# Performance work log

Measured on AMD Instinct MI355X. Metric: run time of the kernel, lower is better.

The kernel has to match this reference:

```python
import jax, jax.numpy as jnp
import numpy as np

TOK, B, DIM, TXT, NT, KS, H = 576, 64, 1024, 512, 1000, 3, 24
SCALE = TXT ** -0.5  # qk_scale = head_dim**-0.5 with head_dim = out_dim = 512


def _layernorm(x, g, b, eps=1e-5):
    m = jnp.mean(x, axis=-1, keepdims=True)
    v = jnp.var(x, axis=-1, keepdims=True)
    return (x - m) * jax.lax.rsqrt(v + eps) * g + b


def _cross_attn(q_in, kv, Wq):
    # q_in: [B,tok,DIM] -> q: [B,tok,TXT]; kv: [B,NT,TXT] serves as both K and V
    q = jnp.einsum('btd,de->bte', q_in, Wq)
    attn = jax.nn.softmax(jnp.einsum('bte,bne->btn', q, kv) * SCALE, axis=-1)
    return jnp.einsum('btn,bne->bte', attn, kv)


def _dwconv(z, w):
    # z: [B,1,H,H], w: [1,1,KS,KS], padding KS//2, stride 1
    return jax.lax.conv_general_dilated(
        z, w, window_strides=(1, 1), padding=((KS // 2, KS // 2), (KS // 2, KS // 2)),
        dimension_numbers=('NCHW', 'OIHW', 'NCHW'))


def setup_inputs() -> dict:
    key = jax.random.key(0)
    ks = jax.random.split(key, 6)
    return {
        'x': jax.random.normal(ks[0], (TOK + 1, B, DIM), jnp.float32),
        'text_fea': jax.random.normal(ks[1], (NT, B, TXT), jnp.float32),
        'ln_q1_g': jnp.ones((DIM,), jnp.float32), 'ln_q1_b': jnp.zeros((DIM,), jnp.float32),
        'ln_q2_g': jnp.ones((DIM,), jnp.float32), 'ln_q2_b': jnp.zeros((DIM,), jnp.float32),
        'ln_kv_g': jnp.ones((TXT,), jnp.float32), 'ln_kv_b': jnp.zeros((TXT,), jnp.float32),
        'Wq1': jax.random.normal(ks[2], (DIM, TXT), jnp.float32) * 0.02,
        'Wq2': jax.random.normal(ks[3], (DIM, TXT), jnp.float32) * 0.02,
        'conv_dw': jax.random.normal(ks[4], (1, 1, KS, KS), jnp.float32) * 0.1,
        'conv_final': jax.random.normal(ks[5], (DIM, TXT), jnp.float32) * 0.02,  # [out,in]
    }


def reference(x, text_fea, ln_q1_g, ln_q1_b, ln_q2_g, ln_q2_b, ln_kv_g, ln_kv_b,
              Wq1, Wq2, conv_dw, conv_final):
    x_cls, xp = x[:1], x[1:]                      # [1,B,DIM], [TOK,B,DIM]
    x_loc = jnp.transpose(xp, (1, 0, 2))          # [B,TOK,DIM]
    kv = _layernorm(jnp.transpose(text_fea, (1, 0, 2)), ln_kv_g, ln_kv_b)  # [B,NT,TXT]

    o1 = _cross_attn(_layernorm(x_loc, ln_q1_g, ln_q1_b), kv, Wq1)  # [B,TOK,TXT]
    o2 = _cross_attn(_layernorm(x_loc, ln_q2_g, ln_q2_b), kv, Wq2)

    x1 = jnp.transpose(o1, (0, 2, 1)).reshape(B, TXT, H, H)
    x2 = jnp.transpose(o2, (0, 2, 1)).reshape(B, TXT, H, H)

    avg_x = jnp.mean(x1, axis=1, keepdims=True)   # [B,1,H,H]
    max_x = jnp.max(x2, axis=1, keepdims=True)
    gate1 = jax.nn.sigmoid(_dwconv(avg_x, conv_dw))
    gate2 = jax.nn.sigmoid(_dwconv(max_x, conv_dw))

    x_se = x1 * gate1 + x2 * gate2                # [B,TXT,H,H]
    y = jnp.einsum('bchw,oc->bohw', x_se, conv_final)  # 1x1 conv, padding 0

    y = jnp.transpose(y.reshape(B, DIM, TOK), (2, 0, 1))  # [TOK,B,DIM]
    return jnp.concatenate([x_cls, y], axis=0)
```

## Files before the change

kernel.cpp:

```cpp
#include <hip/hip_runtime.h>

#define B_    64
#define TOK_  576
#define DIM_  1024
#define TXT_  512
#define NT_   1000
#define NTQ_  1024
#define NTP_  1024
#define H_    24
#define BT_   (B_ * TOK_)
static constexpr float SCALE_ = 0.0441941738241592f;

typedef __bf16 bf16x8 __attribute__((ext_vector_type(8)));
typedef float  f32x4  __attribute__((ext_vector_type(4)));

__device__ __forceinline__ unsigned short f2bf(float f) {
    unsigned u = __float_as_uint(f);
    u += 0x7fffu + ((u >> 16) & 1u);
    return (unsigned short)(u >> 16);
}
__device__ __forceinline__ float bf2f(unsigned short h) {
    return __uint_as_float(((unsigned)h) << 16);
}
__device__ __forceinline__ f32x4 mfma16(bf16x8 a, bf16x8 b, f32x4 c) {
    return __builtin_amdgcn_mfma_f32_16x16x32_bf16(a, b, c, 0, 0, 0);
}
__device__ __forceinline__ void unpack8(uint4 v, float* f) {
    unsigned a0 = v.x, a1 = v.y, a2 = v.z, a3 = v.w;
    f[0] = bf2f((unsigned short)(a0 & 0xffff)); f[1] = bf2f((unsigned short)(a0 >> 16));
    f[2] = bf2f((unsigned short)(a1 & 0xffff)); f[3] = bf2f((unsigned short)(a1 >> 16));
    f[4] = bf2f((unsigned short)(a2 & 0xffff)); f[5] = bf2f((unsigned short)(a2 >> 16));
    f[6] = bf2f((unsigned short)(a3 & 0xffff)); f[7] = bf2f((unsigned short)(a3 >> 16));
}

typedef const __attribute__((address_space(1))) unsigned int* as1_u32p;
typedef __attribute__((address_space(3))) unsigned int* as3_u32p;
__device__ __forceinline__ void gll16(const void* g, void* l) {
    __builtin_amdgcn_global_load_lds((as1_u32p)g, (as3_u32p)l, 16, 0, 0);
}

__global__ void k_prep_wq(const float* __restrict__ wq1, const float* __restrict__ wq2,
                          const float* __restrict__ g1, const float* __restrict__ g2,
                          unsigned short* __restrict__ wqt) {
    __shared__ float tile[64][68];
    int bx = blockIdx.x, t = threadIdx.x;
    int br = bx >> 7, kt = (bx >> 3) & 15, nt = bx & 7;
    const float* wq = br ? wq2 : wq1;
    const float* gg = br ? g2 : g1;
#pragma unroll
    for (int i = 0; i < 4; ++i) {
        int idx4 = t + i * 256;
        int kl = idx4 >> 4, n4 = (idx4 & 15) * 4;
        float gv = gg[kt * 64 + kl];
        float4 v = *reinterpret_cast<const float4*>(wq + (size_t)(kt * 64 + kl) * 512 + nt * 64 + n4);
        tile[kl][n4 + 0] = v.x * gv; tile[kl][n4 + 1] = v.y * gv;
        tile[kl][n4 + 2] = v.z * gv; tile[kl][n4 + 3] = v.w * gv;
    }
    __syncthreads();
#pragma unroll
    for (int i = 0; i < 4; ++i) {
        int idx4 = t + i * 256;
        int nl = idx4 >> 4, k4 = (idx4 & 15) * 4;
        ushort4 o = make_ushort4(f2bf(tile[k4 + 0][nl]), f2bf(tile[k4 + 1][nl]),
                                 f2bf(tile[k4 + 2][nl]), f2bf(tile[k4 + 3][nl]));
        *reinterpret_cast<ushort4*>(wqt + (size_t)br * 512 * 1024 + (size_t)(nt * 64 + nl) * 1024 + kt * 64 + k4) = o;
    }
}

__global__ void k_qbias(const float* __restrict__ wq1, const float* __restrict__ wq2,
                        const float* __restrict__ b1, const float* __restrict__ b2,
                        float* __restrict__ qbias) {
    int br = blockIdx.x >> 3, e0 = (blockIdx.x & 7) * 64;
    int t = threadIdx.x;
    int e = e0 + (t & 63), part = t >> 6;
    const float* wq = br ? wq2 : wq1;
    const float* bb = br ? b2 : b1;
    float s = 0.f;
    for (int d = part * 256; d < part * 256 + 256; ++d) s += bb[d] * wq[(size_t)d * 512 + e];
    __shared__ float red[256];
    red[t] = s;
    __syncthreads();
    if (t < 64) qbias[br * 512 + e0 + t] = red[t] + red[64 + t] + red[128 + t] + red[192 + t];
}

__global__ void k_f2bf(const float* __restrict__ src, unsigned short* __restrict__ dst, int n4) {
    int i = blockIdx.x * blockDim.x + threadIdx.x;
    if (i < n4) {
        float4 v = *reinterpret_cast<const float4*>(src + (size_t)i * 4);
        ushort4 o = make_ushort4(f2bf(v.x), f2bf(v.y), f2bf(v.z), f2bf(v.w));
        *reinterpret_cast<ushort4*>(dst + (size_t)i * 4) = o;
    }
}

__global__ void k_kvln(const float* __restrict__ tf, const float* __restrict__ g,
                       const float* __restrict__ bta, unsigned short* __restrict__ kvn) {
    int row = blockIdx.x;
    int b = row >> 10, n = row & 1023;
    int t = threadIdx.x;
    unsigned short* dst = kvn + ((size_t)b * NTQ_ + n) * TXT_;
    if (n >= NT_) {
        *reinterpret_cast<ushort4*>(dst + t * 4) = make_ushort4(0, 0, 0, 0);
        return;
    }
    const float* src = tf + ((size_t)n * B_ + b) * TXT_;
    float4 v = *reinterpret_cast<const float4*>(src + t * 4);
    float s = v.x + v.y + v.z + v.w;
    float ss = v.x * v.x + v.y * v.y + v.z * v.z + v.w * v.w;
#pragma unroll
    for (int d = 1; d < 64; d <<= 1) { s += __shfl_xor(s, d); ss += __shfl_xor(ss, d); }
    __shared__ float red[4];
    if ((t & 63) == 0) { red[(t >> 6) * 2] = s; red[(t >> 6) * 2 + 1] = ss; }
    __syncthreads();
    s = red[0] + red[2]; ss = red[1] + red[3];
    float m = s * (1.f / TXT_);
    float rs = rsqrtf(ss * (1.f / TXT_) - m * m + 1e-5f);
    int d0 = t * 4;
    ushort4 o = make_ushort4(f2bf((v.x - m) * rs * g[d0 + 0] + bta[d0 + 0]),
                             f2bf((v.y - m) * rs * g[d0 + 1] + bta[d0 + 1]),
                             f2bf((v.z - m) * rs * g[d0 + 2] + bta[d0 + 2]),
                             f2bf((v.w - m) * rs * g[d0 + 3] + bta[d0 + 3]));
    *reinterpret_cast<ushort4*>(dst + d0) = o;
}

__global__ void k_kvt(const unsigned short* __restrict__ kvn, unsigned short* __restrict__ kvt) {
    __shared__ unsigned short tile[64][68];
    int bx = blockIdx.x;
    int b = bx >> 7, rem = bx & 127, et = rem >> 4, nt = rem & 15;
    int t = threadIdx.x;
#pragma unroll
    for (int i = 0; i < 4; ++i) {
        int idx4 = t + i * 256;
        int nl = idx4 >> 4, e4 = (idx4 & 15) * 4;
        int ng = nt * 64 + nl;
        ushort4 v = make_ushort4(0, 0, 0, 0);
        if (ng < NT_) v = *reinterpret_cast<const ushort4*>(kvn + ((size_t)b * NTQ_ + ng) * TXT_ + et * 64 + e4);
        tile[nl][e4 + 0] = v.x; tile[nl][e4 + 1] = v.y; tile[nl][e4 + 2] = v.z; tile[nl][e4 + 3] = v.w;
    }
    __syncthreads();
#pragma unroll
    for (int i = 0; i < 4; ++i) {
        int idx4 = t + i * 256;
        int el = idx4 >> 4, n4 = (idx4 & 15) * 4;
        ushort4 o = make_ushort4(tile[n4 + 0][el], tile[n4 + 1][el], tile[n4 + 2][el], tile[n4 + 3][el]);
        *reinterpret_cast<ushort4*>(kvt + ((size_t)b * TXT_ + et * 64 + el) * NTP_ + nt * 64 + n4) = o;
    }
}

__global__ void k_xln(const float* __restrict__ x, unsigned short* __restrict__ xn) {
    int bt = blockIdx.x;
    int b = bt / TOK_, tk = bt - b * TOK_;
    const float* src = x + ((size_t)(tk + 1) * B_ + b) * DIM_;
    int t = threadIdx.x;
    float4 v = *reinterpret_cast<const float4*>(src + t * 4);
    float s = v.x + v.y + v.z + v.w;
    float ss = v.x * v.x + v.y * v.y + v.z * v.z + v.w * v.w;
#pragma unroll
    for (int d = 1; d < 64; d <<= 1) { s += __shfl_xor(s, d); ss += __shfl_xor(ss, d); }
    __shared__ float red[8];
    if ((t & 63) == 0) { red[t >> 6] = s; red[4 + (t >> 6)] = ss; }
    __syncthreads();
    s = red[0] + red[1] + red[2] + red[3];
    ss = red[4] + red[5] + red[6] + red[7];
    float m = s * (1.f / DIM_);
    float rs = rsqrtf(ss * (1.f / DIM_) - m * m + 1e-5f);
    int d0 = t * 4;
    ushort4 o = make_ushort4(f2bf((v.x - m) * rs), f2bf((v.y - m) * rs),
                             f2bf((v.z - m) * rs), f2bf((v.w - m) * rs));
    *reinterpret_cast<ushort4*>(xn + (size_t)bt * DIM_ + d0) = o;
}

__device__ __forceinline__ void gemm_loop_gll(const unsigned short* __restrict__ A,
                                              const unsigned short* __restrict__ Bp,
                                              int K, unsigned short* a_lds, unsigned short* b_lds,
                                              int tid, f32x4 acc[4][4]) {
    const int l = tid & 63, w = tid >> 6;
    const int l16 = l & 15, lg = l >> 4;
    const int wm = w & 1, wn = w >> 1;
    const f32x4 fz = {0.f, 0.f, 0.f, 0.f};
#pragma unroll
    for (int mt = 0; mt < 4; ++mt)
#pragma unroll
        for (int nt = 0; nt < 4; ++nt) acc[mt][nt] = fz;
    const int lrow = l >> 3;
    const int k8g = (l & 7) ^ lrow;
    const int nk = K >> 6;
    for (int kt = 0; kt < nk; ++kt) {
#pragma unroll
        for (int i = 0; i < 4; ++i) {
            int row = i * 32 + w * 8 + lrow;
            gll16(A + (size_t)row * K + kt * 64 + k8g * 8, &a_lds[(i * 256 + w * 64) * 8]);
        }
#pragma unroll
        for (int i = 0; i < 4; ++i) {
            int row = i * 32 + w * 8 + lrow;
            gll16(Bp + (size_t)row * K + kt * 64 + k8g * 8, &b_lds[(i * 256 + w * 64) * 8]);
        }
        __syncthreads();
#pragma unroll
        for (int kk = 0; kk < 2; ++kk) {
            bf16x8 af[4], bff[4];
#pragma unroll
            for (int mt = 0; mt < 4; ++mt) {
                int row = wm * 64 + mt * 16 + l16;
                int gs = (kk * 4 + lg) ^ (row & 7);
                af[mt] = *reinterpret_cast<const bf16x8*>(a_lds + row * 64 + gs * 8);
            }
#pragma unroll
            for (int nt = 0; nt < 4; ++nt) {
                int row = wn * 64 + nt * 16 + l16;
                int gs = (kk * 4 + lg) ^ (row & 7);
                bff[nt] = *reinterpret_cast<const bf16x8*>(b_lds + row * 64 + gs * 8);
            }
#pragma unroll
            for (int mt = 0; mt < 4; ++mt)
#pragma unroll
                for (int nt = 0; nt < 4; ++nt)
                    acc[mt][nt] = mfma16(af[mt], bff[nt], acc[mt][nt]);
        }
        __syncthreads();
    }
}

__device__ __forceinline__ void gemm_loop96(const unsigned short* __restrict__ A,
                                            const unsigned short* __restrict__ Bp,
                                            int K, unsigned short* a_lds, unsigned short* b_lds,
                                            int tid, f32x4 acc[3][4]) {
    const int l = tid & 63, w = tid >> 6;
    const int l16 = l & 15, lg = l >> 4;
    const int wm = w & 1, wn = w >> 1;
    const f32x4 fz = {0.f, 0.f, 0.f, 0.f};
#pragma unroll
    for (int mt = 0; mt < 3; ++mt)
#pragma unroll
        for (int nt = 0; nt < 4; ++nt) acc[mt][nt] = fz;
    const int lrow = l >> 3;
    const int k8g = (l & 7) ^ lrow;
    const int nk = K >> 6;
    for (int kt = 0; kt < nk; ++kt) {
#pragma unroll
        for (int i = 0; i < 3; ++i) {
            int row = i * 32 + w * 8 + lrow;
            gll16(A + (size_t)row * K + kt * 64 + k8g * 8, &a_lds[(i * 256 + w * 64) * 8]);
        }
#pragma unroll
        for (int i = 0; i < 4; ++i) {
            int row = i * 32 + w * 8 + lrow;
            gll16(Bp + (size_t)row * K + kt * 64 + k8g * 8, &b_lds[(i * 256 + w * 64) * 8]);
        }
        __syncthreads();
#pragma unroll
        for (int kk = 0; kk < 2; ++kk) {
            bf16x8 af[3], bff[4];
#pragma unroll
            for (int mt = 0; mt < 3; ++mt) {
                int row = wm * 48 + mt * 16 + l16;
                int gs = (kk * 4 + lg) ^ (row & 7);
                af[mt] = *reinterpret_cast<const bf16x8*>(a_lds + row * 64 + gs * 8);
            }
#pragma unroll
            for (int nt = 0; nt < 4; ++nt) {
                int row = wn * 64 + nt * 16 + l16;
                int gs = (kk * 4 + lg) ^ (row & 7);
                bff[nt] = *reinterpret_cast<const bf16x8*>(b_lds + row * 64 + gs * 8);
            }
#pragma unroll
            for (int mt = 0; mt < 3; ++mt)
#pragma unroll
                for (int nt = 0; nt < 4; ++nt)
                    acc[mt][nt] = mfma16(af[mt], bff[nt], acc[mt][nt]);
        }
        __syncthreads();
    }
}

__global__ __launch_bounds__(256, 4) void k_qgemm(const unsigned short* __restrict__ xn,
                                                  const unsigned short* __restrict__ wqt,
                                                  const float* __restrict__ qbias,
                                                  unsigned short* __restrict__ qb) {
    int bid = blockIdx.x;
    int vb = (bid & 7) * 288 + (bid >> 3);
    int bn = vb & 3;
    int t = vb >> 2;
    int br = (t >= 288) ? 1 : 0;
    int bm = t - br * 288;
    const unsigned short* A = xn + (size_t)bm * 128 * DIM_;
    const unsigned short* Bp = wqt + (size_t)br * 512 * 1024 + (size_t)bn * 128 * 1024;
    unsigned short* C = qb + (size_t)br * BT_ * TXT_;
    const float* bias = qbias + br * 512;
    __shared__ unsigned short a_lds[128 * 64];
    __shared__ unsigned short b_lds[128 * 64];
    f32x4 acc[4][4];
    gemm_loop_gll(A, Bp, DIM_, a_lds, b_lds, threadIdx.x, acc);
    const int l = threadIdx.x & 63, w = threadIdx.x >> 6;
    const int l16 = l & 15, lg = l >> 4, wm = w & 1, wn = w >> 1;
#pragma unroll
    for (int mt = 0; mt < 4; ++mt)
#pragma unroll
        for (int nt = 0; nt < 4; ++nt) {
            int col = bn * 128 + wn * 64 + nt * 16 + l16;
            float bv = bias[col];
#pragma unroll
            for (int r = 0; r < 4; ++r) {
                int row = bm * 128 + wm * 64 + mt * 16 + lg * 4 + r;
                C[(size_t)row * TXT_ + col] = f2bf((acc[mt][nt][r] + bv) * SCALE_);
            }
        }
}

__global__ __launch_bounds__(256, 4) void k_score(const unsigned short* __restrict__ qbuf,
                                                  const unsigned short* __restrict__ kvn,
                                                  unsigned short* __restrict__ P,
                                                  float* __restrict__ denom, int br) {
    int bid = blockIdx.x;
    int vb = (bid & 7) * 384 + (bid >> 3);
    int tile = vb % 48, b = vb / 48;
    int mt = tile >> 3, nt = tile & 7;
    const unsigned short* A = qbuf + ((size_t)br * BT_ + (size_t)b * TOK_ + mt * 96) * TXT_;
    const unsigned short* Bp = kvn + (size_t)b * NTQ_ * TXT_ + (size_t)nt * 128 * TXT_;
    __shared__ unsigned short a_lds[96 * 64];
    __shared__ unsigned short b_lds[128 * 64];
    f32x4 acc[3][4];
    gemm_loop96(A, Bp, TXT_, a_lds, b_lds, threadIdx.x, acc);
    const int l = threadIdx.x & 63, w = threadIdx.x >> 6;
    const int l16 = l & 15, lg = l >> 4, wm = w & 1, wn = w >> 1;
    float* dn = denom + (size_t)br * BT_;
#pragma unroll
    for (int mt2 = 0; mt2 < 3; ++mt2)
#pragma unroll
        for (int r = 0; r < 4; ++r) {
            int row = b * TOK_ + mt * 96 + wm * 48 + mt2 * 16 + lg * 4 + r;
            float s = 0.f;
#pragma unroll
            for (int nt2 = 0; nt2 < 4; ++nt2) {
                int col = nt * 128 + wn * 64 + nt2 * 16 + l16;
                float p = (col < NT_) ? __expf(acc[mt2][nt2][r]) : 0.f;
                s += p;
                P[(size_t)row * NTP_ + col] = f2bf(p);
            }
#pragma unroll
            for (int d = 1; d < 16; d <<= 1) s += __shfl_xor(s, d);
            if (l16 == 0) atomicAdd(&dn[row], s);
        }
}

__global__ __launch_bounds__(256, 4) void k_pv(const unsigned short* __restrict__ P,
                                               const unsigned short* __restrict__ kvt,
                                               const float* __restrict__ denom,
                                               unsigned short* __restrict__ ob, int br) {
    int bid = blockIdx.x;
    int vb = (bid & 7) * 192 + (bid >> 3);
    int tile = vb % 24, b = vb / 24;
    int mt = tile >> 2, nt = tile & 3;
    const unsigned short* A = P + ((size_t)b * TOK_ + mt * 96) * NTP_;
    const unsigned short* Bp = kvt + (size_t)b * TXT_ * NTP_ + (size_t)nt * 128 * NTP_;
    __shared__ unsigned short a_lds[96 * 64];
    __shared__ unsigned short b_lds[128 * 64];
    f32x4 acc[3][4];
    gemm_loop96(A, Bp, NTP_, a_lds, b_lds, threadIdx.x, acc);
    const int l = threadIdx.x & 63, w = threadIdx.x >> 6;
    const int l16 = l & 15, lg = l >> 4, wm = w & 1, wn = w >> 1;
    const float* dn = denom + (size_t)br * BT_;
#pragma unroll
    for (int mt2 = 0; mt2 < 3; ++mt2)
#pragma unroll
        for (int r = 0; r < 4; ++r) {
            int row = b * TOK_ + mt * 96 + wm * 48 + mt2 * 16 + lg * 4 + r;
            float inv = 1.f / dn[row];
            unsigned short* dst = ob + ((size_t)br * BT_ + row) * TXT_;
#pragma unroll
            for (int nt2 = 0; nt2 < 4; ++nt2) {
                int col = nt * 128 + wn * 64 + nt2 * 16 + l16;
                dst[col] = f2bf(acc[mt2][nt2][r] * inv);
            }
        }
}

__global__ __launch_bounds__(256, 4) void k_fgemm(const unsigned short* __restrict__ xse,
                                                  const unsigned short* __restrict__ wfb,
                                                  float* __restrict__ out) {
    int bid = blockIdx.x;
    int vb = (bid & 7) * 288 + (bid >> 3);
    int bn = vb & 7, bm = vb >> 3;
    const unsigned short* A = xse + (size_t)bm * 128 * TXT_;
    const unsigned short* Bp = wfb + (size_t)bn * 128 * TXT_;
    __shared__ unsigned short a_lds[128 * 64];
    __shared__ unsigned short b_lds[128 * 64];
    f32x4 acc[4][4];
    gemm_loop_gll(A, Bp, TXT_, a_lds, b_lds, threadIdx.x, acc);
    const int l = threadIdx.x & 63, w = threadIdx.x >> 6;
    const int l16 = l & 15, lg = l >> 4, wm = w & 1, wn = w >> 1;
#pragma unroll
    for (int mt = 0; mt < 4; ++mt)
#pragma unroll
        for (int r = 0; r < 4; ++r) {
            int rowg = bm * 128 + wm * 64 + mt * 16 + lg * 4 + r;
            int b = rowg / TOK_, tk = rowg - b * TOK_;
            float* dst = out + ((size_t)(tk + 1) * B_ + b) * DIM_;
#pragma unroll
            for (int nt = 0; nt < 4; ++nt) {
                int col = bn * 128 + wn * 64 + nt * 16 + l16;
                dst[col] = acc[mt][nt][r];
            }
        }
}

__global__ void k_avgmax(const unsigned short* __restrict__ o1, const unsigned short* __restrict__ o2,
                         float* __restrict__ avgb, float* __restrict__ maxb) {
    int row = blockIdx.x * 4 + (threadIdx.x >> 6);
    int l = threadIdx.x & 63;
    float f[8];
    unpack8(*reinterpret_cast<const uint4*>(o1 + (size_t)row * TXT_ + l * 8), f);
    float s = f[0] + f[1] + f[2] + f[3] + f[4] + f[5] + f[6] + f[7];
    unpack8(*reinterpret_cast<const uint4*>(o2 + (size_t)row * TXT_ + l * 8), f);
    float mx = f[0];
#pragma unroll
    for (int j = 1; j < 8; ++j) mx = fmaxf(mx, f[j]);
#pragma unroll
    for (int d = 1; d < 64; d <<= 1) { s += __shfl_xor(s, d); mx = fmaxf(mx, __shfl_xor(mx, d)); }
    if (l == 0) { avgb[row] = s * (1.f / TXT_); maxb[row] = mx; }
}

__global__ void k_gate(const float* __restrict__ avgb, const float* __restrict__ maxb,
                       const float* __restrict__ cdw, float* __restrict__ g1, float* __restrict__ g2) {
    int idx = blockIdx.x * 256 + threadIdx.x;
    int b = idx / TOK_, hw = idx - b * TOK_, h = hw / H_, ww = hw - h * H_;
    float a1 = 0.f, a2 = 0.f;
#pragma unroll
    for (int ky = 0; ky < 3; ++ky)
#pragma unroll
        for (int kx = 0; kx < 3; ++kx) {
            int hh = h + ky - 1, wx = ww + kx - 1;
            if (hh >= 0 && hh < H_ && wx >= 0 && wx < H_) {
                float wv = cdw[ky * 3 + kx];
                int s = b * TOK_ + hh * H_ + wx;
                a1 += wv * avgb[s];
                a2 += wv * maxb[s];
            }
        }
    g1[idx] = 1.f / (1.f + __expf(-a1));
    g2[idx] = 1.f / (1.f + __expf(-a2));
}

__global__ void k_xse(const unsigned short* __restrict__ o1, const unsigned short* __restrict__ o2,
                      const float* __restrict__ g1, const float* __restrict__ g2,
                      unsigned short* __restrict__ xse) {
    int idx8 = blockIdx.x * 256 + threadIdx.x;
    int bt = idx8 >> 6, e8 = idx8 & 63;
    float f1[8], f2[8];
    unpack8(*reinterpret_cast<const uint4*>(o1 + (size_t)bt * TXT_ + e8 * 8), f1);
    unpack8(*reinterpret_cast<const uint4*>(o2 + (size_t)bt * TXT_ + e8 * 8), f2);
    float gg1 = g1[bt], gg2 = g2[bt];
    unsigned r[4];
#pragma unroll
    for (int j = 0; j < 4; ++j) {
        unsigned lo = f2bf(f1[2 * j] * gg1 + f2[2 * j] * gg2);
        unsigned hi = f2bf(f1[2 * j + 1] * gg1 + f2[2 * j + 1] * gg2);
        r[j] = lo | (hi << 16);
    }
    uint4 o = make_uint4(r[0], r[1], r[2], r[3]);
    *reinterpret_cast<uint4*>(xse + (size_t)bt * TXT_ + e8 * 8) = o;
}

extern "C" void kernel_launch(void* const* d_in, const int* in_sizes, int n_in,
                              void* d_out, int out_size, void* d_ws, size_t ws_size,
                              hipStream_t stream) {
    (void)in_sizes; (void)n_in; (void)out_size; (void)ws_size;
    const float* x    = (const float*)d_in[0];
    const float* tf   = (const float*)d_in[1];
    const float* lq1g = (const float*)d_in[2];
    const float* lq1b = (const float*)d_in[3];
    const float* lq2g = (const float*)d_in[4];
    const float* lq2b = (const float*)d_in[5];
    const float* lkvg = (const float*)d_in[6];
    const float* lkvb = (const float*)d_in[7];
    const float* wq1  = (const float*)d_in[8];
    const float* wq2  = (const float*)d_in[9];
    const float* cdw  = (const float*)d_in[10];
    const float* wf   = (const float*)d_in[11];
    float* out = (float*)d_out;

    char* ws = (char*)d_ws;
    size_t off = 0;
    auto carve = [&](size_t bytes) { char* p = ws + off; off += (bytes + 255) & ~(size_t)255; return p; };
    unsigned short* kvn  = (unsigned short*)carve((size_t)B_ * NTQ_ * TXT_ * 2);
    unsigned short* kvt  = (unsigned short*)carve((size_t)B_ * TXT_ * NTP_ * 2);
    unsigned short* wqt  = (unsigned short*)carve((size_t)2 * 512 * 1024 * 2);
    unsigned short* wfb  = (unsigned short*)carve((size_t)1024 * 512 * 2);
    float* qbias = (float*)carve((size_t)2 * 512 * 4);
    float* denom = (float*)carve((size_t)2 * BT_ * 4);
    float* avgb = (float*)carve((size_t)BT_ * 4);
    float* maxb = (float*)carve((size_t)BT_ * 4);
    float* g1v  = (float*)carve((size_t)BT_ * 4);
    float* g2v  = (float*)carve((size_t)BT_ * 4);
    unsigned short* xn   = (unsigned short*)carve((size_t)BT_ * DIM_ * 2);
    unsigned short* qbuf = (unsigned short*)carve((size_t)2 * BT_ * TXT_ * 2);
    unsigned short* ob   = (unsigned short*)carve((size_t)2 * BT_ * TXT_ * 2);
    unsigned short* Pm   = xn;
    unsigned short* xse  = qbuf;

    hipMemcpyAsync(out, x, (size_t)B_ * DIM_ * sizeof(float), hipMemcpyDeviceToDevice, stream);

    k_prep_wq<<<256, 256, 0, stream>>>(wq1, wq2, lq1g, lq2g, wqt);
    k_qbias<<<16, 256, 0, stream>>>(wq1, wq2, lq1b, lq2b, qbias);
    k_f2bf<<<512, 256, 0, stream>>>(wf, wfb, 131072);
    k_kvln<<<B_ * NTQ_, 128, 0, stream>>>(tf, lkvg, lkvb, kvn);
    k_kvt<<<8192, 256, 0, stream>>>(kvn, kvt);
    k_xln<<<BT_, 256, 0, stream>>>(x, xn);
    k_qgemm<<<2304, 256, 0, stream>>>(xn, wqt, qbias, qbuf);
    hipMemsetAsync(denom, 0, (size_t)2 * BT_ * 4, stream);
    k_score<<<3072, 256, 0, stream>>>(qbuf, kvn, Pm, denom, 0);
    k_pv<<<1536, 256, 0, stream>>>(Pm, kvt, denom, ob, 0);
    k_score<<<3072, 256, 0, stream>>>(qbuf, kvn, Pm, denom, 1);
    k_pv<<<1536, 256, 0, stream>>>(Pm, kvt, denom, ob, 1);
    k_avgmax<<<9216, 256, 0, stream>>>(ob, ob + (size_t)BT_ * TXT_, avgb, maxb);
    k_gate<<<144, 256, 0, stream>>>(avgb, maxb, cdw, g1v, g2v);
    k_xse<<<9216, 256, 0, stream>>>(ob, ob + (size_t)BT_ * TXT_, g1v, g2v, xse);
    k_fgemm<<<2304, 256, 0, stream>>>(xse, wfb, out);
}
```

Measured before the change: 608.3 us.

## Fuse KV layernorm with transpose and fold avg/max/gate into PV and xse

Merges the KV layernorm and transpose kernels into one that normalizes 32 rows per block and writes both the row-major and the transposed bf16 copies, so the extra kvn re-read is gone. The PV epilogue now reduces each row's channel sum (branch 0) or max (branch 1) and accumulates it into global buffers with atomics, using an order-preserving integer encoding for the max. The 3x3 conv and sigmoid gating move into k_xse. This removes the avgmax and gate kernels and one full pass over the attention outputs, at the cost of atomic traffic, two extra memsets, and redundant gate computation per row.

New measurement: 792.2 us. +30.2%, slower.

```diff
diff --git a/kernel.cpp b/kernel.cpp
--- a/kernel.cpp
+++ b/kernel.cpp
@@ -31,6 +31,14 @@
     f[2] = bf2f((unsigned short)(a1 & 0xffff)); f[3] = bf2f((unsigned short)(a1 >> 16));
     f[4] = bf2f((unsigned short)(a2 & 0xffff)); f[5] = bf2f((unsigned short)(a2 >> 16));
     f[6] = bf2f((unsigned short)(a3 & 0xffff)); f[7] = bf2f((unsigned short)(a3 >> 16));
+}
+__device__ __forceinline__ unsigned encmax(float f) {
+    unsigned u = __float_as_uint(f);
+    return (u & 0x80000000u) ? ~u : (u | 0x80000000u);
+}
+__device__ __forceinline__ float decmax(unsigned k) {
+    unsigned u = (k & 0x80000000u) ? (k ^ 0x80000000u) : ~k;
+    return __uint_as_float(u);
 }
 
 typedef const __attribute__((address_space(1))) unsigned int* as1_u32p;
@@ -92,57 +100,70 @@
     }
 }
 
-__global__ void k_kvln(const float* __restrict__ tf, const float* __restrict__ g,
-                       const float* __restrict__ bta, unsigned short* __restrict__ kvn) {
-    int row = blockIdx.x;
-    int b = row >> 10, n = row & 1023;
-    int t = threadIdx.x;
-    unsigned short* dst = kvn + ((size_t)b * NTQ_ + n) * TXT_;
-    if (n >= NT_) {
-        *reinterpret_cast<ushort4*>(dst + t * 4) = make_ushort4(0, 0, 0, 0);
-        return;
-    }
-    const float* src = tf + ((size_t)n * B_ + b) * TXT_;
-    float4 v = *reinterpret_cast<const float4*>(src + t * 4);
-    float s = v.x + v.y + v.z + v.w;
-    float ss = v.x * v.x + v.y * v.y + v.z * v.z + v.w * v.w;
-#pragma unroll
-    for (int d = 1; d < 64; d <<= 1) { s += __shfl_xor(s, d); ss += __shfl_xor(ss, d); }
-    __shared__ float red[4];
-    if ((t & 63) == 0) { red[(t >> 6) * 2] = s; red[(t >> 6) * 2 + 1] = ss; }
+__global__ __launch_bounds__(256, 4) void k_kvlnt(const float* __restrict__ tf,
+                                                  const float* __restrict__ g,
+                                                  const float* __restrict__ bta,
+                                                  unsigned short* __restrict__ kvn,
+                                                  unsigned short* __restrict__ kvt) {
+    __shared__ unsigned short tile[32][514];
+    __shared__ float red[32][8][2];
+    __shared__ float stat[32][2];
+    int b = blockIdx.x >> 5, n0 = (blockIdx.x & 31) * 32;
+    int t = threadIdx.x, r = t >> 3, p = t & 7;
+    int n = n0 + r;
+    bool valid = n < NT_;
+    const float* src = tf + ((size_t)n * B_ + b) * TXT_ + p * 64;
+    float s = 0.f, ss = 0.f;
+    if (valid) {
+#pragma unroll
+        for (int j = 0; j < 16; ++j) {
+            float4 v = *reinterpret_cast<const float4*>(src + j * 4);
+            s += v.x + v.y + v.z + v.w;
+            ss += v.x * v.x + v.y * v.y + v.z * v.z + v.w * v.w;
+        }
+    }
+    red[r][p][0] = s; red[r][p][1] = ss;
     __syncthreads();
-    s = red[0] + red[2]; ss = red[1] + red[3];
-    float m = s * (1.f / TXT_);
-    float rs = rsqrtf(ss * (1.f / TXT_) - m * m + 1e-5f);
-    int d0 = t * 4;
-    ushort4 o = make_ushort4(f2bf((v.x - m) * rs * g[d0 + 0] + bta[d0 + 0]),
-                             f2bf((v.y - m) * rs * g[d0 + 1] + bta[d0 + 1]),
-                             f2bf((v.z - m) * rs * g[d0 + 2] + bta[d0 + 2]),
-                             f2bf((v.w - m) * rs * g[d0 + 3] + bta[d0 + 3]));
-    *reinterpret_cast<ushort4*>(dst + d0) = o;
-}
-
-__global__ void k_kvt(const unsigned short* __restrict__ kvn, unsigned short* __restrict__ kvt) {
-    __shared__ unsigned short tile[64][68];
-    int bx = blockIdx.x;
-    int b = bx >> 7, rem = bx & 127, et = rem >> 4, nt = rem & 15;
-    int t = threadIdx.x;
-#pragma unroll
-    for (int i = 0; i < 4; ++i) {
-        int idx4 = t + i * 256;
-        int nl = idx4 >> 4, e4 = (idx4 & 15) * 4;
-        int ng = nt * 64 + nl;
-        ushort4 v = make_ushort4(0, 0, 0, 0);
-        if (ng < NT_) v = *reinterpret_cast<const ushort4*>(kvn + ((size_t)b * NTQ_ + ng) * TXT_ + et * 64 + e4);
-        tile[nl][e4 + 0] = v.x; tile[nl][e4 + 1] = v.y; tile[nl][e4 + 2] = v.z; tile[nl][e4 + 3] = v.w;
+    if (p == 0) {
+        float S = 0.f, SS = 0.f;
+#pragma unroll
+        for (int k = 0; k < 8; ++k) { S += red[r][k][0]; SS += red[r][k][1]; }
+        float m = S * (1.f / TXT_);
+        stat[r][0] = m;
+        stat[r][1] = rsqrtf(SS * (1.f / TXT_) - m * m + 1e-5f);
     }
     __syncthreads();
-#pragma unroll
-    for (int i = 0; i < 4; ++i) {
-        int idx4 = t + i * 256;
-        int el = idx4 >> 4, n4 = (idx4 & 15) * 4;
-        ushort4 o = make_ushort4(tile[n4 + 0][el], tile[n4 + 1][el], tile[n4 + 2][el], tile[n4 + 3][el]);
-        *reinterpret_cast<ushort4*>(kvt + ((size_t)b * TXT_ + et * 64 + el) * NTP_ + nt * 64 + n4) = o;
+    float m = stat[r][0], rs = stat[r][1];
+    unsigned short* dstn = kvn + ((size_t)b * NTQ_ + n) * TXT_ + p * 64;
+#pragma unroll
+    for (int j = 0; j < 16; ++j) {
+        int e = p * 64 + j * 4;
+        unsigned short h0 = 0, h1 = 0, h2 = 0, h3 = 0;
+        if (valid) {
+            float4 v = *reinterpret_cast<const float4*>(src + j * 4);
+            float4 gv = *reinterpret_cast<const float4*>(g + e);
+            float4 bv = *reinterpret_cast<const float4*>(bta + e);
+            h0 = f2bf((v.x - m) * rs * gv.x + bv.x);
+            h1 = f2bf((v.y - m) * rs * gv.y + bv.y);
+            h2 = f2bf((v.z - m) * rs * gv.z + bv.z);
+            h3 = f2bf((v.w - m) * rs * gv.w + bv.w);
+        }
+        *reinterpret_cast<ushort4*>(dstn + j * 4) = make_ushort4(h0, h1, h2, h3);
+        unsigned* tw = reinterpret_cast<unsigned*>(&tile[r][e]);
+        tw[0] = (unsigned)h0 | ((unsigned)h1 << 16);
+        tw[1] = (unsigned)h2 | ((unsigned)h3 << 16);
+    }
+    __syncthreads();
+#pragma unroll
+    for (int ee = 0; ee < 2; ++ee) {
+        int e = ee * 256 + t;
+        unsigned short* dstt = kvt + ((size_t)b * TXT_ + e) * NTP_ + n0;
+#pragma unroll
+        for (int j4 = 0; j4 < 8; ++j4) {
+            ushort4 o = make_ushort4(tile[j4 * 4 + 0][e], tile[j4 * 4 + 1][e],
+                                     tile[j4 * 4 + 2][e], tile[j4 * 4 + 3][e]);
+            *reinterpret_cast<ushort4*>(dstt + j4 * 4) = o;
+        }
     }
 }
 
@@ -346,7 +367,9 @@
 __global__ __launch_bounds__(256, 4) void k_pv(const unsigned short* __restrict__ P,
                                                const unsigned short* __restrict__ kvt,
                                                const float* __restrict__ denom,
-                                               unsigned short* __restrict__ ob, int br) {
+                                               unsigned short* __restrict__ ob,
+                                               float* __restrict__ avgs,
+                                               unsigned* __restrict__ maxe, int br) {
     int bid = blockIdx.x;
     int vb = (bid & 7) * 192 + (bid >> 3);
     int tile = vb % 24, b = vb / 24;
@@ -367,10 +390,23 @@
             int row = b * TOK_ + mt * 96 + wm * 48 + mt2 * 16 + lg * 4 + r;
             float inv = 1.f / dn[row];
             unsigned short* dst = ob + ((size_t)br * BT_ + row) * TXT_;
+            float sum = 0.f, mx = -1e30f;
 #pragma unroll
             for (int nt2 = 0; nt2 < 4; ++nt2) {
                 int col = nt * 128 + wn * 64 + nt2 * 16 + l16;
-                dst[col] = f2bf(acc[mt2][nt2][r] * inv);
+                float o = acc[mt2][nt2][r] * inv;
+                dst[col] = f2bf(o);
+                sum += o;
+                mx = fmaxf(mx, o);
+            }
+#pragma unroll
+            for (int d = 1; d < 16; d <<= 1) {
+                sum += __shfl_xor(sum, d);
+                mx = fmaxf(mx, __shfl_xor(mx, d));
+            }
+            if (l16 == 0) {
+                if (br == 0) atomicAdd(&avgs[row], sum);
+                else         atomicMax(&maxe[row], encmax(mx));
             }
         }
 }
@@ -404,52 +440,35 @@
         }
 }
 
-__global__ void k_avgmax(const unsigned short* __restrict__ o1, const unsigned short* __restrict__ o2,
-                         float* __restrict__ avgb, float* __restrict__ maxb) {
-    int row = blockIdx.x * 4 + (threadIdx.x >> 6);
-    int l = threadIdx.x & 63;
-    float f[8];
-    unpack8(*reinterpret_cast<const uint4*>(o1 + (size_t)row * TXT_ + l * 8), f);
-    float s = f[0] + f[1] + f[2] + f[3] + f[4] + f[5] + f[6] + f[7];
-    unpack8(*reinterpret_cast<const uint4*>(o2 + (size_t)row * TXT_ + l * 8), f);
-    float mx = f[0];
-#pragma unroll
-    for (int j = 1; j < 8; ++j) mx = fmaxf(mx, f[j]);
-#pragma unroll
-    for (int d = 1; d < 64; d <<= 1) { s += __shfl_xor(s, d); mx = fmaxf(mx, __shfl_xor(mx, d)); }
-    if (l == 0) { avgb[row] = s * (1.f / TXT_); maxb[row] = mx; }
-}
-
-__global__ void k_gate(const float* __restrict__ avgb, const float* __restrict__ maxb,
-                       const float* __restrict__ cdw, float* __restrict__ g1, float* __restrict__ g2) {
-    int idx = blockIdx.x * 256 + threadIdx.x;
-    int b = idx / TOK_, hw = idx - b * TOK_, h = hw / H_, ww = hw - h * H_;
-    float a1 = 0.f, a2 = 0.f;
-#pragma unroll
-    for (int ky = 0; ky < 3; ++ky)
-#pragma unroll
-        for (int kx = 0; kx < 3; ++kx) {
-            int hh = h + ky - 1, wx = ww + kx - 1;
-            if (hh >= 0 && hh < H_ && wx >= 0 && wx < H_) {
-                float wv = cdw[ky * 3 + kx];
-                int s = b * TOK_ + hh * H_ + wx;
-                a1 += wv * avgb[s];
-                a2 += wv * maxb[s];
-            }
-        }
-    g1[idx] = 1.f / (1.f + __expf(-a1));
-    g2[idx] = 1.f / (1.f + __expf(-a2));
-}
-
 __global__ void k_xse(const unsigned short* __restrict__ o1, const unsigned short* __restrict__ o2,
-                      const float* __restrict__ g1, const float* __restrict__ g2,
-                      unsigned short* __restrict__ xse) {
+                      const float* __restrict__ avgs, const unsigned* __restrict__ maxe,
+                      const float* __restrict__ cdw, unsigned short* __restrict__ xse) {
     int idx8 = blockIdx.x * 256 + threadIdx.x;
-    int bt = idx8 >> 6, e8 = idx8 & 63;
+    int bt = idx8 >> 6, e8 = threadIdx.x & 63;
+    float gg1 = 0.f, gg2 = 0.f;
+    if (e8 == 0) {
+        int b = bt / TOK_, hw = bt - b * TOK_, h = hw / H_, ww = hw - h * H_;
+        float a1 = 0.f, a2 = 0.f;
+#pragma unroll
+        for (int ky = 0; ky < 3; ++ky)
+#pragma unroll
+            for (int kx = 0; kx < 3; ++kx) {
+                int hh = h + ky - 1, wx = ww + kx - 1;
+                if (hh >= 0 && hh < H_ && wx >= 0 && wx < H_) {
+                    float wv = cdw[ky * 3 + kx];
+                    int s = b * TOK_ + hh * H_ + wx;
+                    a1 += wv * avgs[s] * (1.f / TXT_);
+                    a2 += wv * decmax(maxe[s]);
+                }
+            }
+        gg1 = 1.f / (1.f + __expf(-a1));
+        gg2 = 1.f / (1.f + __expf(-a2));
+    }
+    gg1 = __shfl(gg1, 0);
+    gg2 = __shfl(gg2, 0);
     float f1[8], f2[8];
     unpack8(*reinterpret_cast<const uint4*>(o1 + (size_t)bt * TXT_ + e8 * 8), f1);
     unpack8(*reinterpret_cast<const uint4*>(o2 + (size_t)bt * TXT_ + e8 * 8), f2);
-    float gg1 = g1[bt], gg2 = g2[bt];
     unsigned r[4];
 #pragma unroll
     for (int j = 0; j < 4; ++j) {
@@ -488,10 +507,8 @@
     unsigned short* wfb  = (unsigned short*)carve((size_t)1024 * 512 * 2);
     float* qbias = (float*)carve((size_t)2 * 512 * 4);
     float* denom = (float*)carve((size_t)2 * BT_ * 4);
-    float* avgb = (float*)carve((size_t)BT_ * 4);
-    float* maxb = (float*)carve((size_t)BT_ * 4);
-    float* g1v  = (float*)carve((size_t)BT_ * 4);
-    float* g2v  = (float*)carve((size_t)BT_ * 4);
+    float* avgs  = (float*)carve((size_t)BT_ * 4);
+    unsigned* maxe = (unsigned*)carve((size_t)BT_ * 4);
     unsigned short* xn   = (unsigned short*)carve((size_t)BT_ * DIM_ * 2);
     unsigned short* qbuf = (unsigned short*)carve((size_t)2 * BT_ * TXT_ * 2);
     unsigned short* ob   = (unsigned short*)carve((size_t)2 * BT_ * TXT_ * 2);
@@ -503,17 +520,16 @@
     k_prep_wq<<<256, 256, 0, stream>>>(wq1, wq2, lq1g, lq2g, wqt);
     k_qbias<<<16, 256, 0, stream>>>(wq1, wq2, lq1b, lq2b, qbias);
     k_f2bf<<<512, 256, 0, stream>>>(wf, wfb, 131072);
-    k_kvln<<<B_ * NTQ_, 128, 0, stream>>>(tf, lkvg, lkvb, kvn);
-    k_kvt<<<8192, 256, 0, stream>>>(kvn, kvt);
+    k_kvlnt<<<2048, 256, 0, stream>>>(tf, lkvg, lkvb, kvn, kvt);
     k_xln<<<BT_, 256, 0, stream>>>(x, xn);
     k_qgemm<<<2304, 256, 0, stream>>>(xn, wqt, qbias, qbuf);
     hipMemsetAsync(denom, 0, (size_t)2 * BT_ * 4, stream);
+    hipMemsetAsync(avgs, 0, (size_t)BT_ * 4, stream);
+    hipMemsetAsync(maxe, 0, (size_t)BT_ * 4, stream);
     k_score<<<3072, 256, 0, stream>>>(qbuf, kvn, Pm, denom, 0);
-    k_pv<<<1536, 256, 0, stream>>>(Pm, kvt, denom, ob, 0);
+    k_pv<<<1536, 256, 0, stream>>>(Pm, kvt, denom, ob, avgs, maxe, 0);
     k_score<<<3072, 256, 0, stream>>>(qbuf, kvn, Pm, denom, 1);
-    k_pv<<<1536, 256, 0, stream>>>(Pm, kvt, denom, ob, 1);
-    k_avgmax<<<9216, 256, 0, stream>>>(ob, ob + (size_t)BT_ * TXT_, avgb, maxb);
-    k_gate<<<144, 256, 0, stream>>>(avgb, maxb, cdw, g1v, g2v);
-    k_xse<<<9216, 256, 0, stream>>>(ob, ob + (size_t)BT_ * TXT_, g1v, g2v, xse);
+    k_pv<<<1536, 256, 0, stream>>>(Pm, kvt, denom, ob, avgs, maxe, 1);
+    k_xse<<<9216, 256, 0, stream>>>(ob, ob + (size_t)BT_ * TXT_, avgs, maxe, cdw, xse);
     k_fgemm<<<2304, 256, 0, stream>>>(xse, wfb, out);
 }
```

## Fuse channel avg/max reductions into PV epilogue and gate conv into xse kernel

Applied to the files above, without the earlier changes.

The PV kernel epilogue now reduces each output row's partial sum (branch 1) or max (branch 2) across its 16 lanes and combines them with float atomicAdd, or atomicMax on an order-preserving unsigned encoding of the float. This removes the k_avgmax pass, which re-read both 2*BT*512 bf16 outputs. The 3x3 depthwise gate conv plus sigmoid is recomputed per row inside k_xse by lane 0 and broadcast with a shuffle, which removes the k_gate launch and its gate buffers. In exchange there are two extra memsets, atomics in the PV epilogue, and sums taken from fp32 values rather than the rounded bf16 outputs, so results can differ slightly.

After: 636.9 us. 1.05x slower.

```diff
diff --git a/kernel.cpp b/kernel.cpp
--- a/kernel.cpp
+++ b/kernel.cpp
@@ -31,6 +31,14 @@
     f[2] = bf2f((unsigned short)(a1 & 0xffff)); f[3] = bf2f((unsigned short)(a1 >> 16));
     f[4] = bf2f((unsigned short)(a2 & 0xffff)); f[5] = bf2f((unsigned short)(a2 >> 16));
     f[6] = bf2f((unsigned short)(a3 & 0xffff)); f[7] = bf2f((unsigned short)(a3 >> 16));
+}
+__device__ __forceinline__ unsigned encmax(float f) {
+    unsigned u = __float_as_uint(f);
+    return (u & 0x80000000u) ? ~u : (u | 0x80000000u);
+}
+__device__ __forceinline__ float decmax(unsigned k) {
+    unsigned u = (k & 0x80000000u) ? (k ^ 0x80000000u) : ~k;
+    return __uint_as_float(u);
 }
 
 typedef const __attribute__((address_space(1))) unsigned int* as1_u32p;
@@ -346,7 +354,9 @@
 __global__ __launch_bounds__(256, 4) void k_pv(const unsigned short* __restrict__ P,
                                                const unsigned short* __restrict__ kvt,
                                                const float* __restrict__ denom,
-                                               unsigned short* __restrict__ ob, int br) {
+                                               unsigned short* __restrict__ ob,
+                                               float* __restrict__ avgs,
+                                               unsigned* __restrict__ maxe, int br) {
     int bid = blockIdx.x;
     int vb = (bid & 7) * 192 + (bid >> 3);
     int tile = vb % 24, b = vb / 24;
@@ -367,10 +377,23 @@
             int row = b * TOK_ + mt * 96 + wm * 48 + mt2 * 16 + lg * 4 + r;
             float inv = 1.f / dn[row];
             unsigned short* dst = ob + ((size_t)br * BT_ + row) * TXT_;
+            float sum = 0.f, mx = -1e30f;
 #pragma unroll
             for (int nt2 = 0; nt2 < 4; ++nt2) {
                 int col = nt * 128 + wn * 64 + nt2 * 16 + l16;
-                dst[col] = f2bf(acc[mt2][nt2][r] * inv);
+                float o = acc[mt2][nt2][r] * inv;
+                dst[col] = f2bf(o);
+                sum += o;
+                mx = fmaxf(mx, o);
+            }
+#pragma unroll
+            for (int d = 1; d < 16; d <<= 1) {
+                sum += __shfl_xor(sum, d);
+                mx = fmaxf(mx, __shfl_xor(mx, d));
+            }
+            if (l16 == 0) {
+                if (br == 0) atomicAdd(&avgs[row], sum);
+                else         atomicMax(&maxe[row], encmax(mx));
             }
         }
 }
@@ -404,52 +427,35 @@
         }
 }
 
-__global__ void k_avgmax(const unsigned short* __restrict__ o1, const unsigned short* __restrict__ o2,
-                         float* __restrict__ avgb, float* __restrict__ maxb) {
-    int row = blockIdx.x * 4 + (threadIdx.x >> 6);
-    int l = threadIdx.x & 63;
-    float f[8];
-    unpack8(*reinterpret_cast<const uint4*>(o1 + (size_t)row * TXT_ + l * 8), f);
-    float s = f[0] + f[1] + f[2] + f[3] + f[4] + f[5] + f[6] + f[7];
-    unpack8(*reinterpret_cast<const uint4*>(o2 + (size_t)row * TXT_ + l * 8), f);
-    float mx = f[0];
-#pragma unroll
-    for (int j = 1; j < 8; ++j) mx = fmaxf(mx, f[j]);
-#pragma unroll
-    for (int d = 1; d < 64; d <<= 1) { s += __shfl_xor(s, d); mx = fmaxf(mx, __shfl_xor(mx, d)); }
-    if (l == 0) { avgb[row] = s * (1.f / TXT_); maxb[row] = mx; }
-}
-
-__global__ void k_gate(const float* __restrict__ avgb, const float* __restrict__ maxb,
-                       const float* __restrict__ cdw, float* __restrict__ g1, float* __restrict__ g2) {
-    int idx = blockIdx.x * 256 + threadIdx.x;
-    int b = idx / TOK_, hw = idx - b * TOK_, h = hw / H_, ww = hw - h * H_;
-    float a1 = 0.f, a2 = 0.f;
-#pragma unroll
-    for (int ky = 0; ky < 3; ++ky)
-#pragma unroll
-        for (int kx = 0; kx < 3; ++kx) {
-            int hh = h + ky - 1, wx = ww + kx - 1;
-            if (hh >= 0 && hh < H_ && wx >= 0 && wx < H_) {
-                float wv = cdw[ky * 3 + kx];
-                int s = b * TOK_ + hh * H_ + wx;
-                a1 += wv * avgb[s];
-                a2 += wv * maxb[s];
-            }
-        }
-    g1[idx] = 1.f / (1.f + __expf(-a1));
-    g2[idx] = 1.f / (1.f + __expf(-a2));
-}
-
 __global__ void k_xse(const unsigned short* __restrict__ o1, const unsigned short* __restrict__ o2,
-                      const float* __restrict__ g1, const float* __restrict__ g2,
-                      unsigned short* __restrict__ xse) {
+                      const float* __restrict__ avgs, const unsigned* __restrict__ maxe,
+                      const float* __restrict__ cdw, unsigned short* __restrict__ xse) {
     int idx8 = blockIdx.x * 256 + threadIdx.x;
-    int bt = idx8 >> 6, e8 = idx8 & 63;
+    int bt = idx8 >> 6, e8 = threadIdx.x & 63;
+    float gg1 = 0.f, gg2 = 0.f;
+    if (e8 == 0) {
+        int b = bt / TOK_, hw = bt - b * TOK_, h = hw / H_, ww = hw - h * H_;
+        float a1 = 0.f, a2 = 0.f;
+#pragma unroll
+        for (int ky = 0; ky < 3; ++ky)
+#pragma unroll
+            for (int kx = 0; kx < 3; ++kx) {
+                int hh = h + ky - 1, wx = ww + kx - 1;
+                if (hh >= 0 && hh < H_ && wx >= 0 && wx < H_) {
+                    float wv = cdw[ky * 3 + kx];
+                    int s = b * TOK_ + hh * H_ + wx;
+                    a1 += wv * avgs[s] * (1.f / TXT_);
+                    a2 += wv * decmax(maxe[s]);
+                }
+            }
+        gg1 = 1.f / (1.f + __expf(-a1));
+        gg2 = 1.f / (1.f + __expf(-a2));
+    }
+    gg1 = __shfl(gg1, 0);
+    gg2 = __shfl(gg2, 0);
     float f1[8], f2[8];
     unpack8(*reinterpret_cast<const uint4*>(o1 + (size_t)bt * TXT_ + e8 * 8), f1);
     unpack8(*reinterpret_cast<const uint4*>(o2 + (size_t)bt * TXT_ + e8 * 8), f2);
-    float gg1 = g1[bt], gg2 = g2[bt];
     unsigned r[4];
 #pragma unroll
     for (int j = 0; j < 4; ++j) {
@@ -488,10 +494,8 @@
     unsigned short* wfb  = (unsigned short*)carve((size_t)1024 * 512 * 2);
     float* qbias = (float*)carve((size_t)2 * 512 * 4);
     float* denom = (float*)carve((size_t)2 * BT_ * 4);
-    float* avgb = (float*)carve((size_t)BT_ * 4);
-    float* maxb = (float*)carve((size_t)BT_ * 4);
-    float* g1v  = (float*)carve((size_t)BT_ * 4);
-    float* g2v  = (float*)carve((size_t)BT_ * 4);
+    float* avgs  = (float*)carve((size_t)BT_ * 4);
+    unsigned* maxe = (unsigned*)carve((size_t)BT_ * 4);
     unsigned short* xn   = (unsigned short*)carve((size_t)BT_ * DIM_ * 2);
     unsigned short* qbuf = (unsigned short*)carve((size_t)2 * BT_ * TXT_ * 2);
     unsigned short* ob   = (unsigned short*)carve((size_t)2 * BT_ * TXT_ * 2);
@@ -508,12 +512,12 @@
     k_xln<<<BT_, 256, 0, stream>>>(x, xn);
     k_qgemm<<<2304, 256, 0, stream>>>(xn, wqt, qbias, qbuf);
     hipMemsetAsync(denom, 0, (size_t)2 * BT_ * 4, stream);
+    hipMemsetAsync(avgs, 0, (size_t)BT_ * 4, stream);
+    hipMemsetAsync(maxe, 0, (size_t)BT_ * 4, stream);
     k_score<<<3072, 256, 0, stream>>>(qbuf, kvn, Pm, denom, 0);
-    k_pv<<<1536, 256, 0, stream>>>(Pm, kvt, denom, ob, 0);
+    k_pv<<<1536, 256, 0, stream>>>(Pm, kvt, denom, ob, avgs, maxe, 0);
     k_score<<<3072, 256, 0, stream>>>(qbuf, kvn, Pm, denom, 1);
-    k_pv<<<1536, 256, 0, stream>>>(Pm, kvt, denom, ob, 1);
-    k_avgmax<<<9216, 256, 0, stream>>>(ob, ob + (size_t)BT_ * TXT_, avgb, maxb);
-    k_gate<<<144, 256, 0, stream>>>(avgb, maxb, cdw, g1v, g2v);
-    k_xse<<<9216, 256, 0, stream>>>(ob, ob + (size_t)BT_ * TXT_, g1v, g2v, xse);
+    k_pv<<<1536, 256, 0, stream>>>(Pm, kvt, denom, ob, avgs, maxe, 1);
+    k_xse<<<9216, 256, 0, stream>>>(ob, ob + (size_t)BT_ * TXT_, avgs, maxe, cdw, xse);
     k_fgemm<<<2304, 256, 0, stream>>>(xse, wfb, out);
 }
```
